# Performance work log

Hardware: AMD Instinct MI355X
Metric: run time of the kernel (lower is better)

Reference implementation:

```python
import jax, jax.numpy as jnp
import numpy as np

EPS = 1e-6
B, K, D = 512, 1024, 256  # batch, out_features, in_features


def setup_inputs() -> dict:
    key = jax.random.key(0)
    kx, kp, ka = jax.random.split(key, 3)
    x = jax.random.normal(kx, (B, D), dtype=jnp.float32)
    # project inputs inside the Poincare ball (norm < 1)
    x = 0.7 * x / (1.0 + jnp.linalg.norm(x, axis=-1, keepdims=True))
    # module inits p, a ~ U(-0.001, 0.001); tiny norms are already inside the ball
    p = jax.random.uniform(kp, (K, D), minval=-0.001, maxval=0.001, dtype=jnp.float32)
    a = jax.random.uniform(ka, (K, D), minval=-0.001, maxval=0.001, dtype=jnp.float32)
    return {"x": x, "p": p, "a": a}


def _mobius_add(u, v):
    # Mobius addition on the Poincare ball (c=1), broadcasting over leading dims
    u2 = jnp.sum(u * u, axis=-1, keepdims=True)
    v2 = jnp.sum(v * v, axis=-1, keepdims=True)
    uv = jnp.sum(u * v, axis=-1, keepdims=True)
    num = (1.0 + 2.0 * uv + v2) * u + (1.0 - u2) * v
    den = 1.0 + 2.0 * uv + u2 * v2
    return num / (den + EPS)


def reference(x, p, a):
    # x: [B, D]; p, a: [K, D]
    p2 = jnp.sum(p * p, axis=-1, keepdims=True)           # [K, 1]
    # parallel transport of a from origin to p: PT_{0->p}(a) = (1 - ||p||^2) a
    a_pt = (1.0 - p2) * a                                  # [K, D]
    lam_p = 2.0 / (1.0 - p2 + EPS)                         # [K, 1] conformal factor at p
    # broadcast hyperplane math instead of materializing .repeat() copies
    z = _mobius_add(-p[None, :, :], x[:, None, :])         # [B, K, D] = (-p) (+) x
    z2 = jnp.sum(z * z, axis=-1)                           # [B, K]
    za = jnp.einsum('bkd,kd->bk', z, a_pt)                 # [B, K]
    na = jnp.linalg.norm(a_pt, axis=-1)                    # [K]
    # Ganea hyperbolic MLR logit: lam_p * ||a|| * asinh(2<z,a> / ((1-||z||^2)||a||))
    logits = lam_p[:, 0][None, :] * na[None, :] * jnp.arcsinh(
        2.0 * za / ((1.0 - z2) * na[None, :] + EPS)
    )
    return logits  # [B, K]
```

## Files before the change

kernel.cpp:

```cpp
#include <hip/hip_runtime.h>
#include <math.h>

#define B_ 512
#define K_ 1024
#define D_ 256
#define EPS_ 1e-6f

#define BM 64
#define BN 32
#define BK 32
#define XLD (BM + 4)
#define PLD (BN + 4)

__global__ __launch_bounds__(256) void hyp_mlr_kernel(
    const float* __restrict__ x,
    const float* __restrict__ p,
    const float* __restrict__ a,
    float* __restrict__ out)
{
    __shared__ __align__(16) float Xs[BK][XLD];
    __shared__ __align__(16) float Ps[BK][PLD];
    __shared__ __align__(16) float As[BK][PLD];

    const int t  = threadIdx.x;
    const int tx = t & 15;
    const int ty = t >> 4;
    const int k0 = blockIdx.x * BN;
    const int b0 = blockIdx.y * BM;

    const int lrow = t >> 3;
    const int lcol = (t & 7) * 4;

    float dotp[4][2] = {{0.f,0.f},{0.f,0.f},{0.f,0.f},{0.f,0.f}};
    float dota[4][2] = {{0.f,0.f},{0.f,0.f},{0.f,0.f},{0.f,0.f}};
    float x2a[4] = {0.f,0.f,0.f,0.f};
    float p2a[2] = {0.f,0.f};
    float a2a[2] = {0.f,0.f};
    float paa[2] = {0.f,0.f};

    for (int kk = 0; kk < D_; kk += BK) {
        __syncthreads();
        {
            float4 v0 = *(const float4*)&x[(b0 + lrow)      * D_ + kk + lcol];
            float4 v1 = *(const float4*)&x[(b0 + lrow + 32) * D_ + kk + lcol];
            Xs[lcol + 0][lrow] = v0.x;
            Xs[lcol + 1][lrow] = v0.y;
            Xs[lcol + 2][lrow] = v0.z;
            Xs[lcol + 3][lrow] = v0.w;
            Xs[lcol + 0][lrow + 32] = v1.x;
            Xs[lcol + 1][lrow + 32] = v1.y;
            Xs[lcol + 2][lrow + 32] = v1.z;
            Xs[lcol + 3][lrow + 32] = v1.w;
        }
        {
            float4 v = *(const float4*)&p[(k0 + lrow) * D_ + kk + lcol];
            Ps[lcol + 0][lrow] = v.x;
            Ps[lcol + 1][lrow] = v.y;
            Ps[lcol + 2][lrow] = v.z;
            Ps[lcol + 3][lrow] = v.w;
        }
        {
            float4 v = *(const float4*)&a[(k0 + lrow) * D_ + kk + lcol];
            As[lcol + 0][lrow] = v.x;
            As[lcol + 1][lrow] = v.y;
            As[lcol + 2][lrow] = v.z;
            As[lcol + 3][lrow] = v.w;
        }
        __syncthreads();

#pragma unroll
        for (int j = 0; j < BK; ++j) {
            float4 xv = *(const float4*)&Xs[j][ty * 4];
            float2 pv = *(const float2*)&Ps[j][tx * 2];
            float2 av = *(const float2*)&As[j][tx * 2];
            float xr[4] = {xv.x, xv.y, xv.z, xv.w};
            float pr[2] = {pv.x, pv.y};
            float ar[2] = {av.x, av.y};
#pragma unroll
            for (int i = 0; i < 4; ++i) {
                x2a[i] = fmaf(xr[i], xr[i], x2a[i]);
#pragma unroll
                for (int c = 0; c < 2; ++c) {
                    dotp[i][c] = fmaf(xr[i], pr[c], dotp[i][c]);
                    dota[i][c] = fmaf(xr[i], ar[c], dota[i][c]);
                }
            }
#pragma unroll
            for (int c = 0; c < 2; ++c) {
                p2a[c] = fmaf(pr[c], pr[c], p2a[c]);
                a2a[c] = fmaf(ar[c], ar[c], a2a[c]);
                paa[c] = fmaf(pr[c], ar[c], paa[c]);
            }
        }
    }

#pragma unroll
    for (int i = 0; i < 4; ++i) {
        const int b = b0 + ty * 4 + i;
        const float x2 = x2a[i];
        float res[2];
#pragma unroll
        for (int c = 0; c < 2; ++c) {
            const float p2 = p2a[c];
            const float a2 = a2a[c];
            const float pa = paa[c];
            const float dt = dotp[i][c];
            const float xa = dota[i][c];

            const float beta  = 1.0f - p2;
            const float alpha = 1.0f + x2 - 2.0f * dt;
            const float den   = 1.0f - 2.0f * dt + p2 * x2;
            const float rg    = 1.0f / (den + EPS_);
            const float z2    = (alpha * alpha * p2 - 2.0f * alpha * beta * dt
                                 + beta * beta * x2) * rg * rg;
            const float za    = beta * (beta * xa - alpha * pa) * rg;
            const float na    = beta * sqrtf(a2);
            const float lam   = 2.0f / (beta + EPS_);
            const float arg   = 2.0f * za / ((1.0f - z2) * na + EPS_);
            res[c] = lam * na * asinhf(arg);
        }
        *(float2*)&out[b * K_ + k0 + tx * 2] = make_float2(res[0], res[1]);
    }
}

extern "C" void kernel_launch(void* const* d_in, const int* in_sizes, int n_in,
                              void* d_out, int out_size, void* d_ws, size_t ws_size,
                              hipStream_t stream) {
    const float* x = (const float*)d_in[0];
    const float* p = (const float*)d_in[1];
    const float* a = (const float*)d_in[2];
    float* out = (float*)d_out;

    dim3 grid(K_ / BN, B_ / BM);
    dim3 block(256);
    hyp_mlr_kernel<<<grid, block, 0, stream>>>(x, p, a, out);
}
```

Before: 76.77 us.

## Double-buffer shared-memory tiles with register prefetch of next K slice

```diff
diff --git a/kernel.cpp b/kernel.cpp
--- a/kernel.cpp
+++ b/kernel.cpp
@@ -18,9 +18,9 @@
     const float* __restrict__ a,
     float* __restrict__ out)
 {
-    __shared__ __align__(16) float Xs[BK][XLD];
-    __shared__ __align__(16) float Ps[BK][PLD];
-    __shared__ __align__(16) float As[BK][PLD];
+    __shared__ __align__(16) float Xs[2][BK][XLD];
+    __shared__ __align__(16) float Ps[2][BK][PLD];
+    __shared__ __align__(16) float As[2][BK][PLD];
 
     const int t  = threadIdx.x;
     const int tx = t & 15;
@@ -31,6 +31,11 @@
     const int lrow = t >> 3;
     const int lcol = (t & 7) * 4;
 
+    const float* xg0 = &x[(b0 + lrow)      * D_ + lcol];
+    const float* xg1 = &x[(b0 + lrow + 32) * D_ + lcol];
+    const float* pg  = &p[(k0 + lrow)      * D_ + lcol];
+    const float* ag  = &a[(k0 + lrow)      * D_ + lcol];
+
     float dotp[4][2] = {{0.f,0.f},{0.f,0.f},{0.f,0.f},{0.f,0.f}};
     float dota[4][2] = {{0.f,0.f},{0.f,0.f},{0.f,0.f},{0.f,0.f}};
     float x2a[4] = {0.f,0.f,0.f,0.f};
@@ -38,41 +43,39 @@
     float a2a[2] = {0.f,0.f};
     float paa[2] = {0.f,0.f};
 
+    {
+        float4 v0 = *(const float4*)&xg0[0];
+        float4 v1 = *(const float4*)&xg1[0];
+        float4 vp = *(const float4*)&pg[0];
+        float4 va = *(const float4*)&ag[0];
+        Xs[0][lcol+0][lrow] = v0.x; Xs[0][lcol+1][lrow] = v0.y;
+        Xs[0][lcol+2][lrow] = v0.z; Xs[0][lcol+3][lrow] = v0.w;
+        Xs[0][lcol+0][lrow+32] = v1.x; Xs[0][lcol+1][lrow+32] = v1.y;
+        Xs[0][lcol+2][lrow+32] = v1.z; Xs[0][lcol+3][lrow+32] = v1.w;
+        Ps[0][lcol+0][lrow] = vp.x; Ps[0][lcol+1][lrow] = vp.y;
+        Ps[0][lcol+2][lrow] = vp.z; Ps[0][lcol+3][lrow] = vp.w;
+        As[0][lcol+0][lrow] = va.x; As[0][lcol+1][lrow] = va.y;
+        As[0][lcol+2][lrow] = va.z; As[0][lcol+3][lrow] = va.w;
+    }
+    __syncthreads();
+
+    int cur = 0;
     for (int kk = 0; kk < D_; kk += BK) {
-        __syncthreads();
-        {
-            float4 v0 = *(const float4*)&x[(b0 + lrow)      * D_ + kk + lcol];
-            float4 v1 = *(const float4*)&x[(b0 + lrow + 32) * D_ + kk + lcol];
-            Xs[lcol + 0][lrow] = v0.x;
-            Xs[lcol + 1][lrow] = v0.y;
-            Xs[lcol + 2][lrow] = v0.z;
-            Xs[lcol + 3][lrow] = v0.w;
-            Xs[lcol + 0][lrow + 32] = v1.x;
-            Xs[lcol + 1][lrow + 32] = v1.y;
-            Xs[lcol + 2][lrow + 32] = v1.z;
-            Xs[lcol + 3][lrow + 32] = v1.w;
+        float4 nv0, nv1, nvp, nva;
+        const bool has_next = (kk + BK) < D_;
+        if (has_next) {
+            const int off = kk + BK;
+            nv0 = *(const float4*)&xg0[off];
+            nv1 = *(const float4*)&xg1[off];
+            nvp = *(const float4*)&pg[off];
+            nva = *(const float4*)&ag[off];
         }
-        {
-            float4 v = *(const float4*)&p[(k0 + lrow) * D_ + kk + lcol];
-            Ps[lcol + 0][lrow] = v.x;
-            Ps[lcol + 1][lrow] = v.y;
-            Ps[lcol + 2][lrow] = v.z;
-            Ps[lcol + 3][lrow] = v.w;
-        }
-        {
-            float4 v = *(const float4*)&a[(k0 + lrow) * D_ + kk + lcol];
-            As[lcol + 0][lrow] = v.x;
-            As[lcol + 1][lrow] = v.y;
-            As[lcol + 2][lrow] = v.z;
-            As[lcol + 3][lrow] = v.w;
-        }
-        __syncthreads();
 
-#pragma unroll
+#pragma unroll 8
         for (int j = 0; j < BK; ++j) {
-            float4 xv = *(const float4*)&Xs[j][ty * 4];
-            float2 pv = *(const float2*)&Ps[j][tx * 2];
-            float2 av = *(const float2*)&As[j][tx * 2];
+            float4 xv = *(const float4*)&Xs[cur][j][ty * 4];
+            float2 pv = *(const float2*)&Ps[cur][j][tx * 2];
+            float2 av = *(const float2*)&As[cur][j][tx * 2];
             float xr[4] = {xv.x, xv.y, xv.z, xv.w};
             float pr[2] = {pv.x, pv.y};
             float ar[2] = {av.x, av.y};
@@ -91,6 +94,20 @@
                 a2a[c] = fmaf(ar[c], ar[c], a2a[c]);
                 paa[c] = fmaf(pr[c], ar[c], paa[c]);
             }
+        }
+
+        if (has_next) {
+            const int nxt = cur ^ 1;
+            Xs[nxt][lcol+0][lrow] = nv0.x; Xs[nxt][lcol+1][lrow] = nv0.y;
+            Xs[nxt][lcol+2][lrow] = nv0.z; Xs[nxt][lcol+3][lrow] = nv0.w;
+            Xs[nxt][lcol+0][lrow+32] = nv1.x; Xs[nxt][lcol+1][lrow+32] = nv1.y;
+            Xs[nxt][lcol+2][lrow+32] = nv1.z; Xs[nxt][lcol+3][lrow+32] = nv1.w;
+            Ps[nxt][lcol+0][lrow] = nvp.x; Ps[nxt][lcol+1][lrow] = nvp.y;
+            Ps[nxt][lcol+2][lrow] = nvp.z; Ps[nxt][lcol+3][lrow] = nvp.w;
+            As[nxt][lcol+0][lrow] = nva.x; As[nxt][lcol+1][lrow] = nva.y;
+            As[nxt][lcol+2][lrow] = nva.z; As[nxt][lcol+3][lrow] = nva.w;
+            __syncthreads();
+            cur = nxt;
         }
     }
 
```

Measured after the change: 79.03 us. +2.9%, slower.

## Split reduction dimension across four thread groups with double-buffered shared tiles

Applied to the files above, without the earlier changes.

```diff
diff --git a/kernel.cpp b/kernel.cpp
--- a/kernel.cpp
+++ b/kernel.cpp
@@ -9,27 +9,48 @@
 #define BM 64
 #define BN 32
 #define BK 32
+#define NG 4
+#define JG (BK / NG)
 #define XLD (BM + 4)
 #define PLD (BN + 4)
 
-__global__ __launch_bounds__(256) void hyp_mlr_kernel(
+__global__ __launch_bounds__(1024) void hyp_mlr_kernel(
     const float* __restrict__ x,
     const float* __restrict__ p,
     const float* __restrict__ a,
     float* __restrict__ out)
 {
-    __shared__ __align__(16) float Xs[BK][XLD];
-    __shared__ __align__(16) float Ps[BK][PLD];
-    __shared__ __align__(16) float As[BK][PLD];
+    __shared__ __align__(16) float Xs[2][BK][XLD];
+    __shared__ __align__(16) float Ps[2][BK][PLD];
+    __shared__ __align__(16) float As[2][BK][PLD];
+    __shared__ float Red[256][27];
 
     const int t  = threadIdx.x;
-    const int tx = t & 15;
-    const int ty = t >> 4;
+    const int u  = t & 255;
+    const int g  = t >> 8;
+    const int tx = u & 15;
+    const int ty = u >> 4;
     const int k0 = blockIdx.x * BN;
     const int b0 = blockIdx.y * BM;
 
-    const int lrow = t >> 3;
-    const int lcol = (t & 7) * 4;
+    int lrow, lcol;
+    const float* gsrc;
+    if (t < 512)      { lrow = t >> 3;          lcol = (t & 7) * 4; gsrc = &x[(b0 + lrow) * D_ + lcol]; }
+    else if (t < 768) { const int q = t - 512;  lrow = q >> 3; lcol = (q & 7) * 4; gsrc = &p[(k0 + lrow) * D_ + lcol]; }
+    else              { const int q = t - 768;  lrow = q >> 3; lcol = (q & 7) * 4; gsrc = &a[(k0 + lrow) * D_ + lcol]; }
+
+    auto stage = [&](int buf, float4 v) {
+        if (t < 512) {
+            Xs[buf][lcol+0][lrow] = v.x; Xs[buf][lcol+1][lrow] = v.y;
+            Xs[buf][lcol+2][lrow] = v.z; Xs[buf][lcol+3][lrow] = v.w;
+        } else if (t < 768) {
+            Ps[buf][lcol+0][lrow] = v.x; Ps[buf][lcol+1][lrow] = v.y;
+            Ps[buf][lcol+2][lrow] = v.z; Ps[buf][lcol+3][lrow] = v.w;
+        } else {
+            As[buf][lcol+0][lrow] = v.x; As[buf][lcol+1][lrow] = v.y;
+            As[buf][lcol+2][lrow] = v.z; As[buf][lcol+3][lrow] = v.w;
+        }
+    };
 
     float dotp[4][2] = {{0.f,0.f},{0.f,0.f},{0.f,0.f},{0.f,0.f}};
     float dota[4][2] = {{0.f,0.f},{0.f,0.f},{0.f,0.f},{0.f,0.f}};
@@ -38,41 +59,21 @@
     float a2a[2] = {0.f,0.f};
     float paa[2] = {0.f,0.f};
 
+    stage(0, *(const float4*)gsrc);
+    __syncthreads();
+
+    int cur = 0;
     for (int kk = 0; kk < D_; kk += BK) {
-        __syncthreads();
-        {
-            float4 v0 = *(const float4*)&x[(b0 + lrow)      * D_ + kk + lcol];
-            float4 v1 = *(const float4*)&x[(b0 + lrow + 32) * D_ + kk + lcol];
-            Xs[lcol + 0][lrow] = v0.x;
-            Xs[lcol + 1][lrow] = v0.y;
-            Xs[lcol + 2][lrow] = v0.z;
-            Xs[lcol + 3][lrow] = v0.w;
-            Xs[lcol + 0][lrow + 32] = v1.x;
-            Xs[lcol + 1][lrow + 32] = v1.y;
-            Xs[lcol + 2][lrow + 32] = v1.z;
-            Xs[lcol + 3][lrow + 32] = v1.w;
-        }
-        {
-            float4 v = *(const float4*)&p[(k0 + lrow) * D_ + kk + lcol];
-            Ps[lcol + 0][lrow] = v.x;
-            Ps[lcol + 1][lrow] = v.y;
-            Ps[lcol + 2][lrow] = v.z;
-            Ps[lcol + 3][lrow] = v.w;
-        }
-        {
-            float4 v = *(const float4*)&a[(k0 + lrow) * D_ + kk + lcol];
-            As[lcol + 0][lrow] = v.x;
-            As[lcol + 1][lrow] = v.y;
-            As[lcol + 2][lrow] = v.z;
-            As[lcol + 3][lrow] = v.w;
-        }
-        __syncthreads();
+        float4 nv;
+        const bool hn = (kk + BK) < D_;
+        if (hn) nv = *(const float4*)(gsrc + kk + BK);
 
 #pragma unroll
-        for (int j = 0; j < BK; ++j) {
-            float4 xv = *(const float4*)&Xs[j][ty * 4];
-            float2 pv = *(const float2*)&Ps[j][tx * 2];
-            float2 av = *(const float2*)&As[j][tx * 2];
+        for (int j = 0; j < JG; ++j) {
+            const int d = g * JG + j;
+            float4 xv = *(const float4*)&Xs[cur][d][ty * 4];
+            float2 pv = *(const float2*)&Ps[cur][d][tx * 2];
+            float2 av = *(const float2*)&As[cur][d][tx * 2];
             float xr[4] = {xv.x, xv.y, xv.z, xv.w};
             float pr[2] = {pv.x, pv.y};
             float ar[2] = {av.x, av.y};
@@ -92,34 +93,73 @@
                 paa[c] = fmaf(pr[c], ar[c], paa[c]);
             }
         }
+
+        if (hn) {
+            stage(cur ^ 1, nv);
+            __syncthreads();
+            cur ^= 1;
+        }
     }
 
+    float pay[26];
 #pragma unroll
     for (int i = 0; i < 4; ++i) {
-        const int b = b0 + ty * 4 + i;
-        const float x2 = x2a[i];
-        float res[2];
+        pay[i * 2 + 0] = dotp[i][0]; pay[i * 2 + 1] = dotp[i][1];
+        pay[8 + i * 2 + 0] = dota[i][0]; pay[8 + i * 2 + 1] = dota[i][1];
+        pay[16 + i] = x2a[i];
+    }
+    pay[20] = p2a[0]; pay[21] = p2a[1];
+    pay[22] = a2a[0]; pay[23] = a2a[1];
+    pay[24] = paa[0]; pay[25] = paa[1];
+
+    __syncthreads();
+    if (g == 1) {
 #pragma unroll
-        for (int c = 0; c < 2; ++c) {
-            const float p2 = p2a[c];
-            const float a2 = a2a[c];
-            const float pa = paa[c];
-            const float dt = dotp[i][c];
-            const float xa = dota[i][c];
+        for (int j = 0; j < 26; ++j) Red[u][j] = pay[j];
+    }
+    __syncthreads();
+    if (g == 2) {
+#pragma unroll
+        for (int j = 0; j < 26; ++j) Red[u][j] += pay[j];
+    }
+    __syncthreads();
+    if (g == 3) {
+#pragma unroll
+        for (int j = 0; j < 26; ++j) Red[u][j] += pay[j];
+    }
+    __syncthreads();
 
-            const float beta  = 1.0f - p2;
-            const float alpha = 1.0f + x2 - 2.0f * dt;
-            const float den   = 1.0f - 2.0f * dt + p2 * x2;
-            const float rg    = 1.0f / (den + EPS_);
-            const float z2    = (alpha * alpha * p2 - 2.0f * alpha * beta * dt
-                                 + beta * beta * x2) * rg * rg;
-            const float za    = beta * (beta * xa - alpha * pa) * rg;
-            const float na    = beta * sqrtf(a2);
-            const float lam   = 2.0f / (beta + EPS_);
-            const float arg   = 2.0f * za / ((1.0f - z2) * na + EPS_);
-            res[c] = lam * na * asinhf(arg);
+    if (g == 0) {
+#pragma unroll
+        for (int j = 0; j < 26; ++j) pay[j] += Red[u][j];
+
+#pragma unroll
+        for (int i = 0; i < 4; ++i) {
+            const int b = b0 + ty * 4 + i;
+            const float x2 = pay[16 + i];
+            float res[2];
+#pragma unroll
+            for (int c = 0; c < 2; ++c) {
+                const float p2 = pay[20 + c];
+                const float a2 = pay[22 + c];
+                const float pa = pay[24 + c];
+                const float dt = pay[i * 2 + c];
+                const float xa = pay[8 + i * 2 + c];
+
+                const float beta  = 1.0f - p2;
+                const float alpha = 1.0f + x2 - 2.0f * dt;
+                const float den   = 1.0f - 2.0f * dt + p2 * x2;
+                const float rg    = 1.0f / (den + EPS_);
+                const float z2    = (alpha * alpha * p2 - 2.0f * alpha * beta * dt
+                                     + beta * beta * x2) * rg * rg;
+                const float za    = beta * (beta * xa - alpha * pa) * rg;
+                const float na    = beta * sqrtf(a2);
+                const float lam   = 2.0f / (beta + EPS_);
+                const float arg   = 2.0f * za / ((1.0f - z2) * na + EPS_);
+                res[c] = lam * na * asinhf(arg);
+            }
+            *(float2*)&out[b * K_ + k0 + tx * 2] = make_float2(res[0], res[1]);
         }
-        *(float2*)&out[b * K_ + k0 + tx * 2] = make_float2(res[0], res[1]);
     }
 }
 
@@ -132,6 +172,6 @@
     float* out = (float*)d_out;
 
     dim3 grid(K_ / BN, B_ / BM);
-    dim3 block(256);
+    dim3 block(1024);
     hyp_mlr_kernel<<<grid, block, 0, stream>>>(x, p, a, out);
 }
```

Result: faster. 71.95 us (-6.3%).

## Use split-bf16 MFMA for dot products with a prep kernel for norms

Applied to the files above, without the earlier changes.

```diff
diff --git a/kernel.cpp b/kernel.cpp
--- a/kernel.cpp
+++ b/kernel.cpp
@@ -6,120 +6,176 @@
 #define D_ 256
 #define EPS_ 1e-6f
 
-#define BM 64
-#define BN 32
-#define BK 32
-#define XLD (BM + 4)
-#define PLD (BN + 4)
+typedef unsigned short u16;
+using bf16x8 = __attribute__((ext_vector_type(8))) short;
+using f32x4  = __attribute__((ext_vector_type(4))) float;
 
-__global__ __launch_bounds__(256) void hyp_mlr_kernel(
-    const float* __restrict__ x,
-    const float* __restrict__ p,
-    const float* __restrict__ a,
+#define XHI_OFF 0
+#define XLO_OFF (512 * 256)
+#define PHI_OFF (2 * 512 * 256)
+#define PLO_OFF (PHI_OFF + 1024 * 256)
+#define AHI_OFF (PLO_OFF + 1024 * 256)
+#define ALO_OFF (AHI_OFF + 1024 * 256)
+#define BF16_TOTAL (ALO_OFF + 1024 * 256)
+#define SCAL_BYTE_OFF (BF16_TOTAL * 2)
+
+__device__ inline u16 bf16_rn(float v) {
+    unsigned u = __float_as_uint(v);
+    unsigned r = u + 0x7FFFu + ((u >> 16) & 1u);
+    return (u16)(r >> 16);
+}
+__device__ inline void split2(float v, u16& h, u16& l) {
+    h = bf16_rn(v);
+    float hf = __uint_as_float(((unsigned)h) << 16);
+    l = bf16_rn(v - hf);
+}
+
+__global__ __launch_bounds__(256) void prep_kernel(
+    const float* __restrict__ x, const float* __restrict__ p,
+    const float* __restrict__ a, u16* __restrict__ wsu,
+    float* __restrict__ scal)
+{
+    const int lane = threadIdx.x & 63;
+    const int rid  = blockIdx.x * 4 + (threadIdx.x >> 6);
+    float* x2 = scal;
+    float* p2 = scal + 512;
+    float* a2 = scal + 512 + 1024;
+    float* pa = scal + 512 + 2048;
+
+    if (rid < 512) {
+        const float4 v = *(const float4*)&x[rid * D_ + lane * 4];
+        ushort4 h, l;
+        split2(v.x, h.x, l.x); split2(v.y, h.y, l.y);
+        split2(v.z, h.z, l.z); split2(v.w, h.w, l.w);
+        *(ushort4*)&wsu[XHI_OFF + rid * D_ + lane * 4] = h;
+        *(ushort4*)&wsu[XLO_OFF + rid * D_ + lane * 4] = l;
+        float s = v.x * v.x + v.y * v.y + v.z * v.z + v.w * v.w;
+#pragma unroll
+        for (int off = 32; off; off >>= 1) s += __shfl_down(s, off);
+        if (lane == 0) x2[rid] = s;
+    } else {
+        const int k = rid - 512;
+        const float4 vp = *(const float4*)&p[k * D_ + lane * 4];
+        const float4 va = *(const float4*)&a[k * D_ + lane * 4];
+        ushort4 hp, lp, ha, la;
+        split2(vp.x, hp.x, lp.x); split2(vp.y, hp.y, lp.y);
+        split2(vp.z, hp.z, lp.z); split2(vp.w, hp.w, lp.w);
+        split2(va.x, ha.x, la.x); split2(va.y, ha.y, la.y);
+        split2(va.z, ha.z, la.z); split2(va.w, ha.w, la.w);
+        *(ushort4*)&wsu[PHI_OFF + k * D_ + lane * 4] = hp;
+        *(ushort4*)&wsu[PLO_OFF + k * D_ + lane * 4] = lp;
+        *(ushort4*)&wsu[AHI_OFF + k * D_ + lane * 4] = ha;
+        *(ushort4*)&wsu[ALO_OFF + k * D_ + lane * 4] = la;
+        float sp = vp.x * vp.x + vp.y * vp.y + vp.z * vp.z + vp.w * vp.w;
+        float sa = va.x * va.x + va.y * va.y + va.z * va.z + va.w * va.w;
+        float sx = vp.x * va.x + vp.y * va.y + vp.z * va.z + vp.w * va.w;
+#pragma unroll
+        for (int off = 32; off; off >>= 1) {
+            sp += __shfl_down(sp, off);
+            sa += __shfl_down(sa, off);
+            sx += __shfl_down(sx, off);
+        }
+        if (lane == 0) { p2[k] = sp; a2[k] = sa; pa[k] = sx; }
+    }
+}
+
+__device__ inline float hyp_logit(float dt, float xa, float x2,
+                                  float p2, float a2, float pav) {
+    const float beta  = 1.0f - p2;
+    const float alpha = 1.0f + x2 - 2.0f * dt;
+    const float den   = 1.0f - 2.0f * dt + p2 * x2;
+    const float rg    = 1.0f / (den + EPS_);
+    const float z2    = (alpha * alpha * p2 - 2.0f * alpha * beta * dt
+                         + beta * beta * x2) * rg * rg;
+    const float za    = beta * (beta * xa - alpha * pav) * rg;
+    const float na    = beta * sqrtf(a2);
+    const float lam   = 2.0f / (beta + EPS_);
+    const float arg   = 2.0f * za / ((1.0f - z2) * na + EPS_);
+    return lam * na * asinhf(arg);
+}
+
+__global__ __launch_bounds__(256) void mfma_kernel(
+    const u16* __restrict__ wsu, const float* __restrict__ scal,
     float* __restrict__ out)
 {
-    __shared__ __align__(16) float Xs[BK][XLD];
-    __shared__ __align__(16) float Ps[BK][PLD];
-    __shared__ __align__(16) float As[BK][PLD];
+    const int lane = threadIdx.x & 63;
+    const int w    = threadIdx.x >> 6;
+    const int l15  = lane & 15;
+    const int quad = lane >> 4;
+    const int b0   = blockIdx.y * 16;
+    const int kw   = blockIdx.x * 128 + w * 32;
 
-    const int t  = threadIdx.x;
-    const int tx = t & 15;
-    const int ty = t >> 4;
-    const int k0 = blockIdx.x * BN;
-    const int b0 = blockIdx.y * BM;
+    const u16* xhi = wsu + XHI_OFF;
+    const u16* xlo = wsu + XLO_OFF;
+    const u16* phi = wsu + PHI_OFF;
+    const u16* plo = wsu + PLO_OFF;
+    const u16* ahi = wsu + AHI_OFF;
+    const u16* alo = wsu + ALO_OFF;
+    const float* x2s = scal;
+    const float* p2s = scal + 512;
+    const float* a2s = scal + 512 + 1024;
+    const float* pas = scal + 512 + 2048;
 
-    const int lrow = t >> 3;
-    const int lcol = (t & 7) * 4;
+    const int arow = b0 + l15;
+    const int kc0  = kw + l15;
+    const int kc1  = kw + 16 + l15;
+    const int dq   = quad * 8;
 
-    float dotp[4][2] = {{0.f,0.f},{0.f,0.f},{0.f,0.f},{0.f,0.f}};
-    float dota[4][2] = {{0.f,0.f},{0.f,0.f},{0.f,0.f},{0.f,0.f}};
-    float x2a[4] = {0.f,0.f,0.f,0.f};
-    float p2a[2] = {0.f,0.f};
-    float a2a[2] = {0.f,0.f};
-    float paa[2] = {0.f,0.f};
+    const u16* xh  = xhi + arow * D_ + dq;
+    const u16* xl  = xlo + arow * D_ + dq;
+    const u16* p0h = phi + kc0 * D_ + dq;
+    const u16* p0l = plo + kc0 * D_ + dq;
+    const u16* a0h = ahi + kc0 * D_ + dq;
+    const u16* a0l = alo + kc0 * D_ + dq;
+    const u16* p1h = phi + kc1 * D_ + dq;
+    const u16* p1l = plo + kc1 * D_ + dq;
+    const u16* a1h = ahi + kc1 * D_ + dq;
+    const u16* a1l = alo + kc1 * D_ + dq;
 
-    for (int kk = 0; kk < D_; kk += BK) {
-        __syncthreads();
-        {
-            float4 v0 = *(const float4*)&x[(b0 + lrow)      * D_ + kk + lcol];
-            float4 v1 = *(const float4*)&x[(b0 + lrow + 32) * D_ + kk + lcol];
-            Xs[lcol + 0][lrow] = v0.x;
-            Xs[lcol + 1][lrow] = v0.y;
-            Xs[lcol + 2][lrow] = v0.z;
-            Xs[lcol + 3][lrow] = v0.w;
-            Xs[lcol + 0][lrow + 32] = v1.x;
-            Xs[lcol + 1][lrow + 32] = v1.y;
-            Xs[lcol + 2][lrow + 32] = v1.z;
-            Xs[lcol + 3][lrow + 32] = v1.w;
-        }
-        {
-            float4 v = *(const float4*)&p[(k0 + lrow) * D_ + kk + lcol];
-            Ps[lcol + 0][lrow] = v.x;
-            Ps[lcol + 1][lrow] = v.y;
-            Ps[lcol + 2][lrow] = v.z;
-            Ps[lcol + 3][lrow] = v.w;
-        }
-        {
-            float4 v = *(const float4*)&a[(k0 + lrow) * D_ + kk + lcol];
-            As[lcol + 0][lrow] = v.x;
-            As[lcol + 1][lrow] = v.y;
-            As[lcol + 2][lrow] = v.z;
-            As[lcol + 3][lrow] = v.w;
-        }
-        __syncthreads();
+    f32x4 accP0 = {0.f, 0.f, 0.f, 0.f};
+    f32x4 accA0 = {0.f, 0.f, 0.f, 0.f};
+    f32x4 accP1 = {0.f, 0.f, 0.f, 0.f};
+    f32x4 accA1 = {0.f, 0.f, 0.f, 0.f};
 
 #pragma unroll
-        for (int j = 0; j < BK; ++j) {
-            float4 xv = *(const float4*)&Xs[j][ty * 4];
-            float2 pv = *(const float2*)&Ps[j][tx * 2];
-            float2 av = *(const float2*)&As[j][tx * 2];
-            float xr[4] = {xv.x, xv.y, xv.z, xv.w};
-            float pr[2] = {pv.x, pv.y};
-            float ar[2] = {av.x, av.y};
-#pragma unroll
-            for (int i = 0; i < 4; ++i) {
-                x2a[i] = fmaf(xr[i], xr[i], x2a[i]);
-#pragma unroll
-                for (int c = 0; c < 2; ++c) {
-                    dotp[i][c] = fmaf(xr[i], pr[c], dotp[i][c]);
-                    dota[i][c] = fmaf(xr[i], ar[c], dota[i][c]);
-                }
-            }
-#pragma unroll
-            for (int c = 0; c < 2; ++c) {
-                p2a[c] = fmaf(pr[c], pr[c], p2a[c]);
-                a2a[c] = fmaf(ar[c], ar[c], a2a[c]);
-                paa[c] = fmaf(pr[c], ar[c], paa[c]);
-            }
-        }
+    for (int dc = 0; dc < 8; ++dc) {
+        const int d = dc * 32;
+        bf16x8 Ah  = *(const bf16x8*)(xh + d);
+        bf16x8 Al  = *(const bf16x8*)(xl + d);
+        bf16x8 P0h = *(const bf16x8*)(p0h + d);
+        bf16x8 P0l = *(const bf16x8*)(p0l + d);
+        bf16x8 B0h = *(const bf16x8*)(a0h + d);
+        bf16x8 B0l = *(const bf16x8*)(a0l + d);
+        bf16x8 P1h = *(const bf16x8*)(p1h + d);
+        bf16x8 P1l = *(const bf16x8*)(p1l + d);
+        bf16x8 B1h = *(const bf16x8*)(a1h + d);
+        bf16x8 B1l = *(const bf16x8*)(a1l + d);
+
+        accP0 = __builtin_amdgcn_mfma_f32_16x16x32_bf16(Ah, P0h, accP0, 0, 0, 0);
+        accP0 = __builtin_amdgcn_mfma_f32_16x16x32_bf16(Ah, P0l, accP0, 0, 0, 0);
+        accP0 = __builtin_amdgcn_mfma_f32_16x16x32_bf16(Al, P0h, accP0, 0, 0, 0);
+
+        accA0 = __builtin_amdgcn_mfma_f32_16x16x32_bf16(Ah, B0h, accA0, 0, 0, 0);
+        accA0 = __builtin_amdgcn_mfma_f32_16x16x32_bf16(Ah, B0l, accA0, 0, 0, 0);
+        accA0 = __builtin_amdgcn_mfma_f32_16x16x32_bf16(Al, B0h, accA0, 0, 0, 0);
+
+        accP1 = __builtin_amdgcn_mfma_f32_16x16x32_bf16(Ah, P1h, accP1, 0, 0, 0);
+        accP1 = __builtin_amdgcn_mfma_f32_16x16x32_bf16(Ah, P1l, accP1, 0, 0, 0);
+        accP1 = __builtin_amdgcn_mfma_f32_16x16x32_bf16(Al, P1h, accP1, 0, 0, 0);
+
+        accA1 = __builtin_amdgcn_mfma_f32_16x16x32_bf16(Ah, B1h, accA1, 0, 0, 0);
+        accA1 = __builtin_amdgcn_mfma_f32_16x16x32_bf16(Ah, B1l, accA1, 0, 0, 0);
+        accA1 = __builtin_amdgcn_mfma_f32_16x16x32_bf16(Al, B1h, accA1, 0, 0, 0);
     }
 
+    const float p2v0 = p2s[kc0], a2v0 = a2s[kc0], pav0 = pas[kc0];
+    const float p2v1 = p2s[kc1], a2v1 = a2s[kc1], pav1 = pas[kc1];
 #pragma unroll
-    for (int i = 0; i < 4; ++i) {
-        const int b = b0 + ty * 4 + i;
-        const float x2 = x2a[i];
-        float res[2];
-#pragma unroll
-        for (int c = 0; c < 2; ++c) {
-            const float p2 = p2a[c];
-            const float a2 = a2a[c];
-            const float pa = paa[c];
-            const float dt = dotp[i][c];
-            const float xa = dota[i][c];
-
-            const float beta  = 1.0f - p2;
-            const float alpha = 1.0f + x2 - 2.0f * dt;
-            const float den   = 1.0f - 2.0f * dt + p2 * x2;
-            const float rg    = 1.0f / (den + EPS_);
-            const float z2    = (alpha * alpha * p2 - 2.0f * alpha * beta * dt
-                                 + beta * beta * x2) * rg * rg;
-            const float za    = beta * (beta * xa - alpha * pa) * rg;
-            const float na    = beta * sqrtf(a2);
-            const float lam   = 2.0f / (beta + EPS_);
-            const float arg   = 2.0f * za / ((1.0f - z2) * na + EPS_);
-            res[c] = lam * na * asinhf(arg);
-        }
-        *(float2*)&out[b * K_ + k0 + tx * 2] = make_float2(res[0], res[1]);
+    for (int r = 0; r < 4; ++r) {
+        const int b = b0 + quad * 4 + r;
+        const float x2v = x2s[b];
+        out[b * K_ + kc0] = hyp_logit(accP0[r], accA0[r], x2v, p2v0, a2v0, pav0);
+        out[b * K_ + kc1] = hyp_logit(accP1[r], accA1[r], x2v, p2v1, a2v1, pav1);
     }
 }
 
@@ -130,8 +186,10 @@
     const float* p = (const float*)d_in[1];
     const float* a = (const float*)d_in[2];
     float* out = (float*)d_out;
+    u16* wsu   = (u16*)d_ws;
+    float* scal = (float*)((char*)d_ws + SCAL_BYTE_OFF);
 
-    dim3 grid(K_ / BN, B_ / BM);
-    dim3 block(256);
-    hyp_mlr_kernel<<<grid, block, 0, stream>>>(x, p, a, out);
+    prep_kernel<<<384, 256, 0, stream>>>(x, p, a, wsu, scal);
+    dim3 g2(8, 32);
+    mfma_kernel<<<g2, 256, 0, stream>>>(wsu, scal, out);
 }
```

New measurement: 72.97 us. 4.9% less time.
